# Kernel tuning notes

Measured on AMD Instinct MI355X. Metric: run time of the kernel, lower is better.

The kernel has to match this reference:

```python
import jax, jax.numpy as jnp
import numpy as np

N_NODES = 50000
N_EDGES = 500000
N_GRAPHS = 512


def _segmean(vals, ids, num):
    # avg aggregation: segment mean with safe divide for empty segments
    s = jax.ops.segment_sum(vals, ids, num_segments=num)
    c = jax.ops.segment_sum(jnp.ones((vals.shape[0], 1), vals.dtype), ids, num_segments=num)
    return s / jnp.maximum(c, 1.0)


def setup_inputs() -> dict:
    key = jax.random.key(0)
    ks = iter(jax.random.split(key, 64))

    def nrm(shape, scale=0.05):
        return jax.random.normal(next(ks), shape, dtype=jnp.float32) * scale

    inp = {}
    inp['x'] = nrm((N_NODES, 64), 1.0)
    inp['e'] = nrm((N_EDGES, 32), 1.0)
    inp['u'] = nrm((N_GRAPHS, 64), 1.0)
    inp['a'] = nrm((N_GRAPHS, 8), 1.0)
    inp['senders'] = jax.random.randint(next(ks), (N_EDGES,), 0, N_NODES)
    inp['receivers'] = jax.random.randint(next(ks), (N_EDGES,), 0, N_NODES)
    inp['node_graph'] = jnp.sort(jax.random.randint(next(ks), (N_NODES,), 0, N_GRAPHS))
    inp['edge_graph'] = jnp.sort(jax.random.randint(next(ks), (N_EDGES,), 0, N_GRAPHS))
    # block 1 (hidden 256)
    inp['We1'] = nrm((32, 256)); inp['be1'] = jnp.zeros((256,), jnp.float32)
    inp['Wn1'] = nrm((64, 256)); inp['Win1'] = nrm((256, 256)); inp['Wout1'] = nrm((256, 256)); inp['bn1'] = jnp.zeros((256,), jnp.float32)
    inp['Wg1'] = nrm((64, 256)); inp['Wgn1'] = nrm((256, 256)); inp['Wge1'] = nrm((256, 256)); inp['bg1'] = jnp.zeros((256,), jnp.float32)
    # block 2 (hidden 128)
    inp['We2'] = nrm((256, 128)); inp['be2'] = jnp.zeros((128,), jnp.float32)
    inp['Wn2'] = nrm((256, 128)); inp['Win2'] = nrm((128, 128)); inp['Wout2'] = nrm((128, 128)); inp['bn2'] = jnp.zeros((128,), jnp.float32)
    inp['Wg2'] = nrm((256, 128)); inp['Wgn2'] = nrm((128, 128)); inp['Wge2'] = nrm((128, 128)); inp['bg2'] = jnp.zeros((128,), jnp.float32)
    # global readout (global_features only)
    inp['Wga'] = nrm((128, 128)); inp['bga'] = jnp.zeros((128,), jnp.float32)
    # action-value MLP: (128 + 8) -> 256 -> 256 -> 1
    inp['Wa1'] = nrm((136, 256)); inp['ba1'] = jnp.zeros((256,), jnp.float32)
    inp['Wa2'] = nrm((256, 256)); inp['ba2'] = jnp.zeros((256,), jnp.float32)
    inp['Wa3'] = nrm((256, 1)); inp['ba3'] = jnp.zeros((1,), jnp.float32)
    return inp


def reference(x, e, u, a, senders, receivers, node_graph, edge_graph,
              We1, be1, Wn1, Win1, Wout1, bn1, Wg1, Wgn1, Wge1, bg1,
              We2, be2, Wn2, Win2, Wout2, bn2, Wg2, Wgn2, Wge2, bg2,
              Wga, bga, Wa1, ba1, Wa2, ba2, Wa3, ba3):
    # --- GraphNetwork block 1 (hidden 256) ---
    e1 = jax.nn.relu(e @ We1 + be1)                                  # [E,256]
    inc1 = _segmean(e1, receivers, N_NODES)                          # avg incoming per node
    out1 = _segmean(e1, senders, N_NODES)                            # avg outgoing per node
    n1 = jax.nn.relu(x @ Wn1 + inc1 @ Win1 + out1 @ Wout1 + bn1)     # [N,256]
    u1 = jax.nn.relu(u @ Wg1 + _segmean(n1, node_graph, N_GRAPHS) @ Wgn1
                     + _segmean(e1, edge_graph, N_GRAPHS) @ Wge1 + bg1)  # [B,256]
    # --- GraphNetwork block 2 (hidden 128) ---
    e2 = jax.nn.relu(e1 @ We2 + be2)                                 # [E,128]
    inc2 = _segmean(e2, receivers, N_NODES)
    out2 = _segmean(e2, senders, N_NODES)
    n2 = jax.nn.relu(n1 @ Wn2 + inc2 @ Win2 + out2 @ Wout2 + bn2)    # [N,128]
    u2 = jax.nn.relu(u1 @ Wg2 + _segmean(n2, node_graph, N_GRAPHS) @ Wgn2
                     + _segmean(e2, edge_graph, N_GRAPHS) @ Wge2 + bg2)  # [B,128]
    # --- global readout + action-value MLP ---
    state_value = u2 @ Wga + bga                                     # [B,128]
    h = jnp.concatenate([state_value, a], axis=1)                    # [B,136]
    h = jax.nn.relu(h @ Wa1 + ba1)
    h = jax.nn.relu(h @ Wa2 + ba2)
    return h @ Wa3 + ba3                                             # [B,1]
```

## Files before the change

### kernel.cpp

```cpp
#include <hip/hip_runtime.h>
#include <hip/hip_bf16.h>

#define N_NODES 50000
#define N_EDGES 500000
#define N_GRAPHS 512

#define FXS16 2048.0f
#define FXI16 4.8828125e-4f

__device__ __forceinline__ unsigned long long pk16x4(float4 v) {
    const unsigned long long a = (unsigned int)fmaf(v.x, FXS16, 0.5f);
    const unsigned long long b = (unsigned int)fmaf(v.y, FXS16, 0.5f);
    const unsigned long long c = (unsigned int)fmaf(v.z, FXS16, 0.5f);
    const unsigned long long d = (unsigned int)fmaf(v.w, FXS16, 0.5f);
    return a | (b << 16) | (c << 32) | (d << 48);
}

typedef __attribute__((ext_vector_type(8))) short bf16x8;
typedef __attribute__((ext_vector_type(4))) float f32x4;

__global__ __launch_bounds__(256) void prep_kernel(
    const float* __restrict__ We2,  const float* __restrict__ Wn1,
    const float* __restrict__ Win1, const float* __restrict__ Wout1,
    const float* __restrict__ Wn2,  const float* __restrict__ Win2,
    const float* __restrict__ Wout2, const float* __restrict__ We1,
    __hip_bfloat16* __restrict__ Wt2,  __hip_bfloat16* __restrict__ Wn1t,
    __hip_bfloat16* __restrict__ Win1t,__hip_bfloat16* __restrict__ Wout1t,
    __hip_bfloat16* __restrict__ Wn2t, __hip_bfloat16* __restrict__ Win2t,
    __hip_bfloat16* __restrict__ Wout2t, __hip_bfloat16* __restrict__ We1t)
{
    const int b = blockIdx.x, t = threadIdx.x;
    const float* src; __hip_bfloat16* dst; int K, N, base;
    if (b < 128)      { src = We2;   dst = Wt2;    K = 256; N = 128; base = 0; }
    else if (b < 192) { src = Wn1;   dst = Wn1t;   K = 64;  N = 256; base = 128; }
    else if (b < 448) { src = Win1;  dst = Win1t;  K = 256; N = 256; base = 192; }
    else if (b < 704) { src = Wout1; dst = Wout1t; K = 256; N = 256; base = 448; }
    else if (b < 832) { src = Wn2;   dst = Wn2t;   K = 256; N = 128; base = 704; }
    else if (b < 896) { src = Win2;  dst = Win2t;  K = 128; N = 128; base = 832; }
    else if (b < 960) { src = Wout2; dst = Wout2t; K = 128; N = 128; base = 896; }
    else              { src = We1;   dst = We1t;   K = 32;  N = 256; base = 960; }
    const int i = (b - base) * 256 + t;
    const int n = i / K, k = i - n * K;
    dst[i] = __float2bfloat16(src[(size_t)k * N + n]);
}

__global__ __launch_bounds__(256) void convert_e_kernel(
    const float* __restrict__ e, __hip_bfloat16* __restrict__ ebf)
{
    const long i = (long)blockIdx.x * 256 + threadIdx.x;
    if (i * 8 >= (long)N_EDGES * 32) return;
    const float4 v0 = *(const float4*)&e[i * 8];
    const float4 v1 = *(const float4*)&e[i * 8 + 4];
    __hip_bfloat16* d = &ebf[i * 8];
    *(__hip_bfloat162*)&d[0] = __float22bfloat162_rn(make_float2(v0.x, v0.y));
    *(__hip_bfloat162*)&d[2] = __float22bfloat162_rn(make_float2(v0.z, v0.w));
    *(__hip_bfloat162*)&d[4] = __float22bfloat162_rn(make_float2(v1.x, v1.y));
    *(__hip_bfloat162*)&d[6] = __float22bfloat162_rn(make_float2(v1.z, v1.w));
}


#define NTILES 196

__global__ __launch_bounds__(256) void count_kernel(
    const int* __restrict__ senders, const int* __restrict__ receivers,
    unsigned int* __restrict__ rc, unsigned int* __restrict__ sc)
{
    const int i = blockIdx.x * 256 + threadIdx.x;
    if (i < N_EDGES) {
        atomicAdd(&rc[receivers[i]], 1u);
        atomicAdd(&sc[senders[i]], 1u);
    }
}

__global__ __launch_bounds__(256) void scan_tile_sum(
    const unsigned int* __restrict__ rc, const unsigned int* __restrict__ sc,
    unsigned int* __restrict__ tsR, unsigned int* __restrict__ tsS)
{
    const int b = blockIdx.x;
    const int sel = (b >= NTILES);
    const int tile = sel ? b - NTILES : b;
    const unsigned int* src = sel ? sc : rc;
    unsigned int* ts = sel ? tsS : tsR;
    const int t = threadIdx.x;
    const int i = tile * 256 + t;
    unsigned int v = (i < N_NODES) ? src[i] : 0u;
    __shared__ unsigned int s[256];
    s[t] = v; __syncthreads();
    for (int off = 128; off > 0; off >>= 1) {
        if (t < off) s[t] += s[t + off];
        __syncthreads();
    }
    if (t == 0) ts[tile] = s[0];
}

__global__ __launch_bounds__(256) void scan_tile_offsets(
    unsigned int* __restrict__ tsR, unsigned int* __restrict__ tsS,
    int* __restrict__ roff, int* __restrict__ soff)
{
    __shared__ unsigned int s[256];
    const int t = threadIdx.x;
    for (int sel = 0; sel < 2; sel++) {
        unsigned int* ts = sel ? tsS : tsR;
        int* off = sel ? soff : roff;
        unsigned int v = (t < NTILES) ? ts[t] : 0u;
        s[t] = v; __syncthreads();
        for (int o = 1; o < 256; o <<= 1) {
            unsigned int x = (t >= o) ? s[t - o] : 0u;
            __syncthreads();
            s[t] += x;
            __syncthreads();
        }
        const unsigned int incl = s[t];
        if (t < NTILES) ts[t] = incl - v;
        if (t == NTILES - 1) off[N_NODES] = (int)incl;
        __syncthreads();
    }
}

__global__ __launch_bounds__(256) void scan_finalize(
    const unsigned int* __restrict__ rc, const unsigned int* __restrict__ sc,
    const unsigned int* __restrict__ tsR, const unsigned int* __restrict__ tsS,
    int* __restrict__ roff, int* __restrict__ soff,
    unsigned int* __restrict__ wpR, unsigned int* __restrict__ wpS)
{
    const int b = blockIdx.x;
    const int sel = (b >= NTILES);
    const int tile = sel ? b - NTILES : b;
    const unsigned int* src = sel ? sc : rc;
    const unsigned int* ts = sel ? tsS : tsR;
    int* off = sel ? soff : roff;
    unsigned int* wp = sel ? wpS : wpR;
    const int t = threadIdx.x, i = tile * 256 + t;
    unsigned int v = (i < N_NODES) ? src[i] : 0u;
    __shared__ unsigned int s[256];
    s[t] = v; __syncthreads();
    for (int o = 1; o < 256; o <<= 1) {
        unsigned int x = (t >= o) ? s[t - o] : 0u;
        __syncthreads();
        s[t] += x;
        __syncthreads();
    }
    const unsigned int excl = s[t] - v + ts[tile];
    if (i < N_NODES) { off[i] = (int)excl; wp[i] = excl; }
}

__global__ __launch_bounds__(256) void csr_fill(
    const int* __restrict__ senders, const int* __restrict__ receivers,
    unsigned int* __restrict__ wpR, unsigned int* __restrict__ wpS,
    int* __restrict__ csrR, int* __restrict__ csrS)
{
    const int i = blockIdx.x * 256 + threadIdx.x;
    if (i < N_EDGES) {
        csrR[atomicAdd(&wpR[receivers[i]], 1u)] = i;
        csrS[atomicAdd(&wpS[senders[i]], 1u)] = i;
    }
}

#define EPB 32
#define EBP 40
#define E1P 264
#define E2P 132

__global__ __launch_bounds__(256) void edge_kernel_e2(
    const float* __restrict__ e,
    const int* __restrict__ edge_graph,
    const __hip_bfloat16* __restrict__ We1t, const float* __restrict__ be1,
    const __hip_bfloat16* __restrict__ Wt2,
    const float* __restrict__ be2,
    float* __restrict__ ge1, float* __restrict__ ge2, float* __restrict__ gecnt)
{
    __shared__ __hip_bfloat16 eB[EPB * EBP];
    __shared__ __hip_bfloat16 e1B[EPB * E1P];
    __shared__ float e2L[EPB * E2P];
    __shared__ int gidx[EPB];

    const int t = threadIdx.x;
    const long e0 = (long)blockIdx.x * EPB;

    {
        const int j = t >> 3, c4 = (t & 7) * 4;
        const float4 v = *(const float4*)&e[(e0 + j) * 32 + c4];
        __hip_bfloat16* d = &eB[j * EBP + c4];
        *(__hip_bfloat162*)&d[0] = __float22bfloat162_rn(make_float2(v.x, v.y));
        *(__hip_bfloat162*)&d[2] = __float22bfloat162_rn(make_float2(v.z, v.w));
    }
    if (t < EPB) gidx[t] = edge_graph[e0 + t];
    __syncthreads();

    const int wv = t >> 6, ln = t & 63;
    const int r0 = ln & 15, q = ln >> 4;

    #pragma unroll
    for (int mt = 0; mt < 2; mt++) {
        const bf16x8 a = *(const bf16x8*)&eB[(mt * 16 + r0) * EBP + q * 8];
        #pragma unroll
        for (int nn = 0; nn < 4; nn++) {
            const int n = (wv * 4 + nn) * 16 + r0;
            const bf16x8 wb = *(const bf16x8*)&We1t[(size_t)n * 32 + q * 8];
            f32x4 c = {0.f, 0.f, 0.f, 0.f};
            c = __builtin_amdgcn_mfma_f32_16x16x32_bf16(a, wb, c, 0, 0, 0);
            const float bz = be1[n];
            #pragma unroll
            for (int r = 0; r < 4; r++)
                e1B[(mt * 16 + q * 4 + r) * E1P + n] =
                    __float2bfloat16(fmaxf(c[r] + bz, 0.f));
        }
    }
    __syncthreads();

    {
        f32x4 acc[2][2] = {{{0.f,0.f,0.f,0.f},{0.f,0.f,0.f,0.f}},
                           {{0.f,0.f,0.f,0.f},{0.f,0.f,0.f,0.f}}};
        const int n0 = (2 * wv) * 16 + r0;
        const int n1 = (2 * wv + 1) * 16 + r0;
        #pragma unroll
        for (int kb = 0; kb < 8; kb++) {
            const int k0 = kb * 32 + q * 8;
            const bf16x8 a0 = *(const bf16x8*)&e1B[(r0) * E1P + k0];
            const bf16x8 a1 = *(const bf16x8*)&e1B[(16 + r0) * E1P + k0];
            const bf16x8 b0 = *(const bf16x8*)&Wt2[(size_t)n0 * 256 + k0];
            const bf16x8 b1 = *(const bf16x8*)&Wt2[(size_t)n1 * 256 + k0];
            acc[0][0] = __builtin_amdgcn_mfma_f32_16x16x32_bf16(a0, b0, acc[0][0], 0, 0, 0);
            acc[0][1] = __builtin_amdgcn_mfma_f32_16x16x32_bf16(a0, b1, acc[0][1], 0, 0, 0);
            acc[1][0] = __builtin_amdgcn_mfma_f32_16x16x32_bf16(a1, b0, acc[1][0], 0, 0, 0);
            acc[1][1] = __builtin_amdgcn_mfma_f32_16x16x32_bf16(a1, b1, acc[1][1], 0, 0, 0);
        }
        const float bz0 = be2[2 * wv * 16 + r0];
        const float bz1 = be2[(2 * wv + 1) * 16 + r0];
        #pragma unroll
        for (int mt = 0; mt < 2; mt++) {
            const int m = mt * 16 + q * 4;
            #pragma unroll
            for (int r = 0; r < 4; r++) {
                e2L[(m + r) * E2P + 2 * wv * 16 + r0]       = fmaxf(acc[mt][0][r] + bz0, 0.f);
                e2L[(m + r) * E2P + (2 * wv + 1) * 16 + r0] = fmaxf(acc[mt][1][r] + bz1, 0.f);
            }
        }
    }
    __syncthreads();

    if (gidx[0] == gidx[EPB - 1]) {
        const int g = gidx[0];
        float s = 0.f;
        #pragma unroll
        for (int j = 0; j < EPB; j++) s += __bfloat162float(e1B[j * E1P + t]);
        atomicAdd(&ge1[(size_t)g * 256 + t], s);
        if (t < 128) {
            float s2 = 0.f;
            #pragma unroll
            for (int j = 0; j < EPB; j++) s2 += e2L[j * E2P + t];
            atomicAdd(&ge2[(size_t)g * 128 + t], s2);
        }
        if (t == 0) atomicAdd(&gecnt[g], (float)EPB);
    } else {
        int j = 0;
        while (j < EPB) {
            const int g = gidx[j];
            int j2 = j;
            float s = 0.f;
            while (j2 < EPB && gidx[j2] == g) { s += __bfloat162float(e1B[j2 * E1P + t]); j2++; }
            atomicAdd(&ge1[(size_t)g * 256 + t], s);
            if (t < 128) {
                float s2 = 0.f;
                for (int jj = j; jj < j2; jj++) s2 += e2L[jj * E2P + t];
                atomicAdd(&ge2[(size_t)g * 128 + t], s2);
            }
            if (t == 0) atomicAdd(&gecnt[g], (float)(j2 - j));
            j = j2;
        }
    }
}

#define ANPB 16
#define CHK 32
#define ESP 40
#define E1CP 312
#define E2CP 184
#define JADDR(j, c, P) ((j) * (P) + (c) + ((((j) >> 3) & 3) << 4))

__global__ __launch_bounds__(256) void agg_kernel(
    const __hip_bfloat16* __restrict__ ebf,
    const int* __restrict__ roff, const int* __restrict__ soff,
    const int* __restrict__ csrR, const int* __restrict__ csrS,
    const __hip_bfloat16* __restrict__ We1t, const float* __restrict__ be1,
    const __hip_bfloat16* __restrict__ Wt2, const float* __restrict__ be2,
    __hip_bfloat16* __restrict__ i1d, __hip_bfloat16* __restrict__ o1d,
    __hip_bfloat16* __restrict__ i2d, __hip_bfloat16* __restrict__ o2d)
{
    __shared__ __hip_bfloat16 eS[CHK * ESP];
    __shared__ __hip_bfloat16 e1C[CHK * E1CP];
    __shared__ __hip_bfloat16 e2C[CHK * E2CP];
    __shared__ int idL[CHK];
    __shared__ int segL[CHK];
    __shared__ int offL[ANPB + 1];

    const int t = threadIdx.x;
    int b = blockIdx.x;
    const int side = (b >= (N_NODES / ANPB));
    if (side) b -= N_NODES / ANPB;
    const int n0 = b * ANPB;
    const int* off = side ? soff : roff;
    const int* lst = side ? csrS : csrR;
    __hip_bfloat16* d1 = side ? o1d : i1d;
    __hip_bfloat16* d2 = side ? o2d : i2d;

    if (t <= ANPB) offL[t] = off[n0 + t];
    __syncthreads();
    const int base = offL[0], end = offL[ANPB];

    const int wv = t >> 6, ln = t & 63;
    const int r0 = ln & 15, q = ln >> 4;

    f32x4 s1[4] = {{0.f,0.f,0.f,0.f},{0.f,0.f,0.f,0.f},
                   {0.f,0.f,0.f,0.f},{0.f,0.f,0.f,0.f}};
    f32x4 s2[2] = {{0.f,0.f,0.f,0.f},{0.f,0.f,0.f,0.f}};

    float bz1[4], bz2[2];
    #pragma unroll
    for (int nn = 0; nn < 4; nn++) bz1[nn] = be1[(wv * 4 + nn) * 16 + r0];
    #pragma unroll
    for (int nn = 0; nn < 2; nn++) bz2[nn] = be2[(wv * 2 + nn) * 16 + r0];

    for (int cb = base; cb < end; cb += CHK) {
        const int cnt = min(CHK, end - cb);
        if (t < CHK) {
            int sg = -1;
            if (t < cnt) {
                const int p = cb + t;
                idL[t] = lst[p];
                sg = 0;
                #pragma unroll
                for (int j = 1; j < ANPB; j++) sg += (p >= offL[j]) ? 1 : 0;
            }
            segL[t] = sg;
        }
        __syncthreads();
        if (t < 128) {
            const int sl = t >> 2, cg = (t & 3) * 8;
            bf16x8 v = {0, 0, 0, 0, 0, 0, 0, 0};
            if (sl < cnt) v = *(const bf16x8*)&ebf[(size_t)idL[sl] * 32 + cg];
            *(bf16x8*)&eS[sl * ESP + cg] = v;
        }
        __syncthreads();

        bf16x8 ind;
        #pragma unroll
        for (int i = 0; i < 8; i++)
            ind[i] = (segL[q * 8 + i] == r0) ? (short)0x3F80 : (short)0;

        #pragma unroll
        for (int mt = 0; mt < 2; mt++) {
            const bf16x8 a = *(const bf16x8*)&eS[(mt * 16 + r0) * ESP + q * 8];
            #pragma unroll
            for (int nn = 0; nn < 4; nn++) {
                const int n = (wv * 4 + nn) * 16 + r0;
                const bf16x8 wb = *(const bf16x8*)&We1t[(size_t)n * 32 + q * 8];
                f32x4 c = {0.f, 0.f, 0.f, 0.f};
                c = __builtin_amdgcn_mfma_f32_16x16x32_bf16(a, wb, c, 0, 0, 0);
                #pragma unroll
                for (int r = 0; r < 4; r++)
                    e1C[JADDR(mt * 16 + q * 4 + r, n, E1CP)] =
                        __float2bfloat16(fmaxf(c[r] + bz1[nn], 0.f));
            }
        }
        __syncthreads();

        #pragma unroll
        for (int nn = 0; nn < 4; nn++) {
            const int n = (wv * 4 + nn) * 16 + r0;
            bf16x8 bfr;
            #pragma unroll
            for (int i = 0; i < 8; i++)
                bfr[i] = *(const short*)&e1C[JADDR(q * 8 + i, n, E1CP)];
            s1[nn] = __builtin_amdgcn_mfma_f32_16x16x32_bf16(ind, bfr, s1[nn], 0, 0, 0);
        }

        #pragma unroll
        for (int mt = 0; mt < 2; mt++) {
            f32x4 c[2] = {{0.f,0.f,0.f,0.f},{0.f,0.f,0.f,0.f}};
            #pragma unroll
            for (int ks = 0; ks < 8; ks++) {
                const bf16x8 a = *(const bf16x8*)&e1C[JADDR(mt * 16 + r0, ks * 32 + q * 8, E1CP)];
                #pragma unroll
                for (int nn = 0; nn < 2; nn++) {
                    const int n = (wv * 2 + nn) * 16 + r0;
                    const bf16x8 wb = *(const bf16x8*)&Wt2[(size_t)n * 256 + ks * 32 + q * 8];
                    c[nn] = __builtin_amdgcn_mfma_f32_16x16x32_bf16(a, wb, c[nn], 0, 0, 0);
                }
            }
            #pragma unroll
            for (int nn = 0; nn < 2; nn++) {
                const int n = (wv * 2 + nn) * 16 + r0;
                #pragma unroll
                for (int r = 0; r < 4; r++)
                    e2C[JADDR(mt * 16 + q * 4 + r, n, E2CP)] =
                        __float2bfloat16(fmaxf(c[nn][r] + bz2[nn], 0.f));
            }
        }
        __syncthreads();

        #pragma unroll
        for (int nn = 0; nn < 2; nn++) {
            const int n = (wv * 2 + nn) * 16 + r0;
            bf16x8 bfr;
            #pragma unroll
            for (int i = 0; i < 8; i++)
                bfr[i] = *(const short*)&e2C[JADDR(q * 8 + i, n, E2CP)];
            s2[nn] = __builtin_amdgcn_mfma_f32_16x16x32_bf16(ind, bfr, s2[nn], 0, 0, 0);
        }
        __syncthreads();
    }

    {
        float inv[4];
        #pragma unroll
        for (int r = 0; r < 4; r++) {
            const int m = q * 4 + r;
            const int deg = offL[m + 1] - offL[m];
            inv[r] = 1.f / (float)(deg > 0 ? deg : 1);
        }
        #pragma unroll
        for (int nn = 0; nn < 4; nn++) {
            const int n = (wv * 4 + nn) * 16 + r0;
            #pragma unroll
            for (int r = 0; r < 4; r++)
                e1C[(q * 4 + r) * E1CP + n] = __float2bfloat16(s1[nn][r] * inv[r]);
        }
        #pragma unroll
        for (int nn = 0; nn < 2; nn++) {
            const int n = (wv * 2 + nn) * 16 + r0;
            #pragma unroll
            for (int r = 0; r < 4; r++)
                e2C[(q * 4 + r) * E2CP + n] = __float2bfloat16(s2[nn][r] * inv[r]);
        }
    }
    __syncthreads();
    for (int i = t; i < ANPB * 32; i += 256) {
        const int j = i >> 5, c8 = (i & 31) * 8;
        *(bf16x8*)&d1[(size_t)(n0 + j) * 256 + c8] = *(const bf16x8*)&e1C[j * E1CP + c8];
    }
    for (int i = t; i < ANPB * 16; i += 256) {
        const int j = i >> 4, c8 = (i & 15) * 8;
        *(bf16x8*)&d2[(size_t)(n0 + j) * 128 + c8] = *(const bf16x8*)&e2C[j * E2CP + c8];
    }
}

#define NPB 16
#define XP  72
#define K1P 264
#define K2P 136

__global__ __launch_bounds__(256) void node_kernel_dense(
    const float* __restrict__ x,
    const int* __restrict__ node_graph,
    const __hip_bfloat16* __restrict__ i1d, const __hip_bfloat16* __restrict__ o1d,
    const __hip_bfloat16* __restrict__ i2d, const __hip_bfloat16* __restrict__ o2d,
    const __hip_bfloat16* __restrict__ Wn1t, const __hip_bfloat16* __restrict__ Win1t,
    const __hip_bfloat16* __restrict__ Wout1t, const float* __restrict__ bn1,
    const __hip_bfloat16* __restrict__ Wn2t, const __hip_bfloat16* __restrict__ Win2t,
    const __hip_bfloat16* __restrict__ Wout2t, const float* __restrict__ bn2,
    float* __restrict__ gn1, float* __restrict__ gn2, float* __restrict__ gncnt)
{
    __shared__ __hip_bfloat16 xB[NPB * XP];
    __shared__ __hip_bfloat16 i1B[NPB * K1P];
    __shared__ __hip_bfloat16 o1B[NPB * K1P];
    __shared__ __hip_bfloat16 i2B[NPB * K2P];
    __shared__ __hip_bfloat16 o2B[NPB * K2P];
    __shared__ __hip_bfloat16 n1B[NPB * K1P];
    __shared__ __hip_bfloat16 n2B[NPB * K2P];
    __shared__ int gI[NPB];

    const int t = threadIdx.x;
    const long n0 = (long)blockIdx.x * NPB;

    if (t < NPB) gI[t] = node_graph[n0 + t];
    for (int i = t; i < NPB * 16; i += 256) {
        const int j = i >> 4, c4 = (i & 15) * 4;
        const float4 v = *(const float4*)&x[(n0 + j) * 64 + c4];
        *(__hip_bfloat162*)&xB[j * XP + c4]     = __float22bfloat162_rn(make_float2(v.x, v.y));
        *(__hip_bfloat162*)&xB[j * XP + c4 + 2] = __float22bfloat162_rn(make_float2(v.z, v.w));
    }
    for (int i = t; i < NPB * 32; i += 256) {
        const int j = i >> 5, c8 = (i & 31) * 8;
        *(bf16x8*)&i1B[j * K1P + c8] = *(const bf16x8*)&i1d[(size_t)(n0 + j) * 256 + c8];
        *(bf16x8*)&o1B[j * K1P + c8] = *(const bf16x8*)&o1d[(size_t)(n0 + j) * 256 + c8];
    }
    for (int i = t; i < NPB * 16; i += 256) {
        const int j = i >> 4, c8 = (i & 15) * 8;
        *(bf16x8*)&i2B[j * K2P + c8] = *(const bf16x8*)&i2d[(size_t)(n0 + j) * 128 + c8];
        *(bf16x8*)&o2B[j * K2P + c8] = *(const bf16x8*)&o2d[(size_t)(n0 + j) * 128 + c8];
    }
    __syncthreads();

    const int wv = t >> 6, ln = t & 63;
    const int r0 = ln & 15, q = ln >> 4;

    {
        f32x4 acc[4] = {{0.f,0.f,0.f,0.f},{0.f,0.f,0.f,0.f},
                        {0.f,0.f,0.f,0.f},{0.f,0.f,0.f,0.f}};
        #pragma unroll
        for (int ks = 0; ks < 2; ks++) {
            const int k0 = ks * 32 + q * 8;
            const bf16x8 a = *(const bf16x8*)&xB[r0 * XP + k0];
            #pragma unroll
            for (int nn = 0; nn < 4; nn++) {
                const int n = (wv * 4 + nn) * 16 + r0;
                const bf16x8 b = *(const bf16x8*)&Wn1t[(size_t)n * 64 + k0];
                acc[nn] = __builtin_amdgcn_mfma_f32_16x16x32_bf16(a, b, acc[nn], 0, 0, 0);
            }
        }
        #pragma unroll
        for (int ks = 0; ks < 8; ks++) {
            const int k0 = ks * 32 + q * 8;
            const bf16x8 a = *(const bf16x8*)&i1B[r0 * K1P + k0];
            #pragma unroll
            for (int nn = 0; nn < 4; nn++) {
                const int n = (wv * 4 + nn) * 16 + r0;
                const bf16x8 b = *(const bf16x8*)&Win1t[(size_t)n * 256 + k0];
                acc[nn] = __builtin_amdgcn_mfma_f32_16x16x32_bf16(a, b, acc[nn], 0, 0, 0);
            }
        }
        #pragma unroll
        for (int ks = 0; ks < 8; ks++) {
            const int k0 = ks * 32 + q * 8;
            const bf16x8 a = *(const bf16x8*)&o1B[r0 * K1P + k0];
            #pragma unroll
            for (int nn = 0; nn < 4; nn++) {
                const int n = (wv * 4 + nn) * 16 + r0;
                const bf16x8 b = *(const bf16x8*)&Wout1t[(size_t)n * 256 + k0];
                acc[nn] = __builtin_amdgcn_mfma_f32_16x16x32_bf16(a, b, acc[nn], 0, 0, 0);
            }
        }
        #pragma unroll
        for (int nn = 0; nn < 4; nn++) {
            const int n = (wv * 4 + nn) * 16 + r0;
            const float bz = bn1[n];
            #pragma unroll
            for (int r = 0; r < 4; r++) {
                const int m = q * 4 + r;
                n1B[m * K1P + n] = __float2bfloat16(fmaxf(acc[nn][r] + bz, 0.f));
            }
        }
    }
    __syncthreads();

    if (gI[0] == gI[NPB - 1]) {
        float s = 0.f;
        #pragma unroll
        for (int j = 0; j < NPB; j++) s += __bfloat162float(n1B[j * K1P + t]);
        atomicAdd(&gn1[(size_t)gI[0] * 256 + t], s);
        if (t == 0) atomicAdd(&gncnt[gI[0]], (float)NPB);
    } else {
        int j = 0;
        while (j < NPB) {
            const int g = gI[j];
            int j2 = j;
            float s = 0.f;
            while (j2 < NPB && gI[j2] == g) { s += __bfloat162float(n1B[j2 * K1P + t]); j2++; }
            atomicAdd(&gn1[(size_t)g * 256 + t], s);
            if (t == 0) atomicAdd(&gncnt[g], (float)(j2 - j));
            j = j2;
        }
    }

    {
        f32x4 acc[2] = {{0.f,0.f,0.f,0.f},{0.f,0.f,0.f,0.f}};
        #pragma unroll
        for (int ks = 0; ks < 8; ks++) {
            const int k0 = ks * 32 + q * 8;
            const bf16x8 a = *(const bf16x8*)&n1B[r0 * K1P + k0];
            #pragma unroll
            for (int nn = 0; nn < 2; nn++) {
                const int n = (wv * 2 + nn) * 16 + r0;
                const bf16x8 b = *(const bf16x8*)&Wn2t[(size_t)n * 256 + k0];
                acc[nn] = __builtin_amdgcn_mfma_f32_16x16x32_bf16(a, b, acc[nn], 0, 0, 0);
            }
        }
        #pragma unroll
        for (int ks = 0; ks < 4; ks++) {
            const int k0 = ks * 32 + q * 8;
            const bf16x8 a = *(const bf16x8*)&i2B[r0 * K2P + k0];
            #pragma unroll
            for (int nn = 0; nn < 2; nn++) {
                const int n = (wv * 2 + nn) * 16 + r0;
                const bf16x8 b = *(const bf16x8*)&Win2t[(size_t)n * 128 + k0];
                acc[nn] = __builtin_amdgcn_mfma_f32_16x16x32_bf16(a, b, acc[nn], 0, 0, 0);
            }
        }
        #pragma unroll
        for (int ks = 0; ks < 4; ks++) {
            const int k0 = ks * 32 + q * 8;
            const bf16x8 a = *(const bf16x8*)&o2B[r0 * K2P + k0];
            #pragma unroll
            for (int nn = 0; nn < 2; nn++) {
                const int n = (wv * 2 + nn) * 16 + r0;
                const bf16x8 b = *(const bf16x8*)&Wout2t[(size_t)n * 128 + k0];
                acc[nn] = __builtin_amdgcn_mfma_f32_16x16x32_bf16(a, b, acc[nn], 0, 0, 0);
            }
        }
        #pragma unroll
        for (int nn = 0; nn < 2; nn++) {
            const int n = (wv * 2 + nn) * 16 + r0;
            const float bz = bn2[n];
            #pragma unroll
            for (int r = 0; r < 4; r++) {
                const int m = q * 4 + r;
                n2B[m * K2P + n] = __float2bfloat16(fmaxf(acc[nn][r] + bz, 0.f));
            }
        }
    }
    __syncthreads();

    if (t < 128) {
        if (gI[0] == gI[NPB - 1]) {
            float s = 0.f;
            #pragma unroll
            for (int j = 0; j < NPB; j++) s += __bfloat162float(n2B[j * K2P + t]);
            atomicAdd(&gn2[(size_t)gI[0] * 128 + t], s);
        } else {
            int j = 0;
            while (j < NPB) {
                const int g = gI[j];
                int j2 = j;
                float s = 0.f;
                while (j2 < NPB && gI[j2] == g) { s += __bfloat162float(n2B[j2 * K2P + t]); j2++; }
                atomicAdd(&gn2[(size_t)g * 128 + t], s);
                j = j2;
            }
        }
    }
}

__global__ __launch_bounds__(256) void graph_kernel(
    const float* __restrict__ u,
    const float* __restrict__ a,
    const float* __restrict__ ge1, const float* __restrict__ ge2,
    const float* __restrict__ gecnt,
    const float* __restrict__ gn1, const float* __restrict__ gn2,
    const float* __restrict__ gncnt,
    const float* __restrict__ Wg1, const float* __restrict__ Wgn1,
    const float* __restrict__ Wge1, const float* __restrict__ bg1,
    const float* __restrict__ Wg2, const float* __restrict__ Wgn2,
    const float* __restrict__ Wge2, const float* __restrict__ bg2,
    const float* __restrict__ Wga, const float* __restrict__ bga,
    const float* __restrict__ Wa1, const float* __restrict__ ba1,
    const float* __restrict__ Wa2, const float* __restrict__ ba2,
    const float* __restrict__ Wa3, const float* __restrict__ ba3,
    float* __restrict__ out)
{
    const int g = blockIdx.x;
    const int t = threadIdx.x;
    __shared__ float uL[64], mn1[256], me1[256], mn2[128], me2[128];
    __shared__ float u1L[256], u2L[128], hL[144], h1L[256], h2L[256];
    __shared__ float red[4];

    const float ec = 1.f / fmaxf(gecnt[g], 1.f);
    const float nc = 1.f / fmaxf(gncnt[g], 1.f);
    if (t < 64) uL[t] = u[(size_t)g * 64 + t];
    mn1[t] = gn1[(size_t)g * 256 + t] * nc;
    me1[t] = ge1[(size_t)g * 256 + t] * ec;
    if (t < 128) {
        mn2[t] = gn2[(size_t)g * 128 + t] * nc;
        me2[t] = ge2[(size_t)g * 128 + t] * ec;
    }
    if (t >= 136 && t < 144) hL[t] = 0.f;
    __syncthreads();

    {
        float acc = bg1[t];
        for (int k = 0; k < 64; k++)  acc = fmaf(uL[k],  Wg1[(size_t)k * 256 + t], acc);
        for (int k = 0; k < 256; k++) acc = fmaf(mn1[k], Wgn1[(size_t)k * 256 + t], acc);
        for (int k = 0; k < 256; k++) acc = fmaf(me1[k], Wge1[(size_t)k * 256 + t], acc);
        u1L[t] = fmaxf(acc, 0.f);
    }
    __syncthreads();
    if (t < 128) {
        float acc = bg2[t];
        for (int k = 0; k < 256; k++) acc = fmaf(u1L[k], Wg2[(size_t)k * 128 + t], acc);
        for (int k = 0; k < 128; k++) acc = fmaf(mn2[k], Wgn2[(size_t)k * 128 + t], acc);
        for (int k = 0; k < 128; k++) acc = fmaf(me2[k], Wge2[(size_t)k * 128 + t], acc);
        u2L[t] = fmaxf(acc, 0.f);
    }
    __syncthreads();
    if (t < 128) {
        float acc = bga[t];
        for (int k = 0; k < 128; k++) acc = fmaf(u2L[k], Wga[(size_t)k * 128 + t], acc);
        hL[t] = acc;
    }
    if (t >= 128 && t < 136) hL[t] = a[(size_t)g * 8 + (t - 128)];
    __syncthreads();
    {
        float acc = ba1[t];
        for (int k = 0; k < 136; k++) acc = fmaf(hL[k], Wa1[(size_t)k * 256 + t], acc);
        h1L[t] = fmaxf(acc, 0.f);
    }
    __syncthreads();
    {
        float acc = ba2[t];
        for (int k = 0; k < 256; k++) acc = fmaf(h1L[k], Wa2[(size_t)k * 256 + t], acc);
        h2L[t] = fmaxf(acc, 0.f);
    }
    __syncthreads();
    {
        float p = h2L[t] * Wa3[t];
        for (int off = 32; off > 0; off >>= 1) p += __shfl_down(p, off, 64);
        if ((t & 63) == 0) red[t >> 6] = p;
        __syncthreads();
        if (t == 0) out[g] = red[0] + red[1] + red[2] + red[3] + ba3[0];
    }
}


__global__ __launch_bounds__(256) void edge_kernel(
// ... 520 lines not shown
```

Baseline: 920.7 us.

## Double-buffer edge gather and widen aggregation chunk to 64 edges

The aggregation kernel now processes 64 edges per chunk instead of 32. It double-buffers the edge ids, segment ids and gathered edge features, so the global gather for the next chunk is issued while the current chunk's MFMA work runs. This is meant to hide global-load latency and cut the number of barriers per edge. In exchange it uses more LDS (the e1C/e2C buffers double in size), which may lower occupancy. Nodes with few edges also waste more of each chunk on padding.

```diff
diff --git a/kernel.cpp b/kernel.cpp
--- a/kernel.cpp
+++ b/kernel.cpp
@@ -272,7 +272,7 @@
 }
 
 #define ANPB 16
-#define CHK 32
+#define CHK 64
 #define ESP 40
 #define E1CP 312
 #define E2CP 184
@@ -287,11 +287,11 @@
     __hip_bfloat16* __restrict__ i1d, __hip_bfloat16* __restrict__ o1d,
     __hip_bfloat16* __restrict__ i2d, __hip_bfloat16* __restrict__ o2d)
 {
-    __shared__ __hip_bfloat16 eS[CHK * ESP];
+    __shared__ __hip_bfloat16 eS[2][CHK * ESP];
     __shared__ __hip_bfloat16 e1C[CHK * E1CP];
     __shared__ __hip_bfloat16 e2C[CHK * E2CP];
-    __shared__ int idL[CHK];
-    __shared__ int segL[CHK];
+    __shared__ int idL[2][CHK];
+    __shared__ int segL[2][CHK];
     __shared__ int offL[ANPB + 1];
 
     const int t = threadIdx.x;
@@ -307,9 +307,11 @@
     if (t <= ANPB) offL[t] = off[n0 + t];
     __syncthreads();
     const int base = offL[0], end = offL[ANPB];
+    const int nchunks = (end - base + CHK - 1) / CHK;
 
     const int wv = t >> 6, ln = t & 63;
     const int r0 = ln & 15, q = ln >> 4;
+    const int srow = t >> 2, scol = (t & 3) * 8;
 
     f32x4 s1[4] = {{0.f,0.f,0.f,0.f},{0.f,0.f,0.f,0.f},
                    {0.f,0.f,0.f,0.f},{0.f,0.f,0.f,0.f}};
@@ -321,63 +323,85 @@
     #pragma unroll
     for (int nn = 0; nn < 2; nn++) bz2[nn] = be2[(wv * 2 + nn) * 16 + r0];
 
-    for (int cb = base; cb < end; cb += CHK) {
-        const int cnt = min(CHK, end - cb);
+    if (t < CHK) {
+        const int p = base + t;
+        int sg = -1, id = 0;
+        if (p < end) {
+            id = lst[p];
+            sg = 0;
+            #pragma unroll
+            for (int j = 1; j < ANPB; j++) sg += (p >= offL[j]) ? 1 : 0;
+        }
+        idL[0][t] = id; segL[0][t] = sg;
+    }
+    __syncthreads();
+    {
+        bf16x8 v = {0, 0, 0, 0, 0, 0, 0, 0};
+        if (segL[0][srow] >= 0) v = *(const bf16x8*)&ebf[(size_t)idL[0][srow] * 32 + scol];
+        *(bf16x8*)&eS[0][srow * ESP + scol] = v;
+    }
+    __syncthreads();
+
+    int cur = 0;
+    for (int c = 0; c < nchunks; c++) {
+        const int nxt = cur ^ 1;
+
+        int idn = 0, sgn = -1;
         if (t < CHK) {
-            int sg = -1;
-            if (t < cnt) {
-                const int p = cb + t;
-                idL[t] = lst[p];
-                sg = 0;
+            const int p = base + (c + 1) * CHK + t;
+            if (c + 1 < nchunks && p < end) {
+                idn = lst[p];
+                sgn = 0;
                 #pragma unroll
-                for (int j = 1; j < ANPB; j++) sg += (p >= offL[j]) ? 1 : 0;
-            }
-            segL[t] = sg;
-        }
-        __syncthreads();
-        if (t < 128) {
-            const int sl = t >> 2, cg = (t & 3) * 8;
-            bf16x8 v = {0, 0, 0, 0, 0, 0, 0, 0};
-            if (sl < cnt) v = *(const bf16x8*)&ebf[(size_t)idL[sl] * 32 + cg];
-            *(bf16x8*)&eS[sl * ESP + cg] = v;
-        }
-        __syncthreads();
-
-        bf16x8 ind;
-        #pragma unroll
-        for (int i = 0; i < 8; i++)
-            ind[i] = (segL[q * 8 + i] == r0) ? (short)0x3F80 : (short)0;
-
-        #pragma unroll
-        for (int mt = 0; mt < 2; mt++) {
-            const bf16x8 a = *(const bf16x8*)&eS[(mt * 16 + r0) * ESP + q * 8];
+                for (int j = 1; j < ANPB; j++) sgn += (p >= offL[j]) ? 1 : 0;
+            }
+        }
+
+        bf16x8 ind[2];
+        #pragma unroll
+        for (int ks = 0; ks < 2; ks++)
+            #pragma unroll
+            for (int i = 0; i < 8; i++)
+                ind[ks][i] = (segL[cur][ks * 32 + q * 8 + i] == r0) ? (short)0x3F80 : (short)0;
+
+        #pragma unroll
+        for (int mt = 0; mt < 4; mt++) {
+            const bf16x8 a = *(const bf16x8*)&eS[cur][(mt * 16 + r0) * ESP + q * 8];
             #pragma unroll
             for (int nn = 0; nn < 4; nn++) {
                 const int n = (wv * 4 + nn) * 16 + r0;
                 const bf16x8 wb = *(const bf16x8*)&We1t[(size_t)n * 32 + q * 8];
-                f32x4 c = {0.f, 0.f, 0.f, 0.f};
-                c = __builtin_amdgcn_mfma_f32_16x16x32_bf16(a, wb, c, 0, 0, 0);
+                f32x4 cc = {0.f, 0.f, 0.f, 0.f};
+                cc = __builtin_amdgcn_mfma_f32_16x16x32_bf16(a, wb, cc, 0, 0, 0);
                 #pragma unroll
                 for (int r = 0; r < 4; r++)
                     e1C[JADDR(mt * 16 + q * 4 + r, n, E1CP)] =
-                        __float2bfloat16(fmaxf(c[r] + bz1[nn], 0.f));
-            }
-        }
+                        __float2bfloat16(fmaxf(cc[r] + bz1[nn], 0.f));
+            }
+        }
+        if (t < CHK) { idL[nxt][t] = idn; segL[nxt][t] = sgn; }
         __syncthreads();
 
-        #pragma unroll
-        for (int nn = 0; nn < 4; nn++) {
-            const int n = (wv * 4 + nn) * 16 + r0;
-            bf16x8 bfr;
-            #pragma unroll
-            for (int i = 0; i < 8; i++)
-                bfr[i] = *(const short*)&e1C[JADDR(q * 8 + i, n, E1CP)];
-            s1[nn] = __builtin_amdgcn_mfma_f32_16x16x32_bf16(ind, bfr, s1[nn], 0, 0, 0);
-        }
-
-        #pragma unroll
-        for (int mt = 0; mt < 2; mt++) {
-            f32x4 c[2] = {{0.f,0.f,0.f,0.f},{0.f,0.f,0.f,0.f}};
+        bf16x8 pre = {0, 0, 0, 0, 0, 0, 0, 0};
+        if (segL[nxt][srow] >= 0)
+            pre = *(const bf16x8*)&ebf[(size_t)idL[nxt][srow] * 32 + scol];
+
+        #pragma unroll
+        for (int ks = 0; ks < 2; ks++) {
+            #pragma unroll
+            for (int nn = 0; nn < 4; nn++) {
+                const int n = (wv * 4 + nn) * 16 + r0;
+                bf16x8 bfr;
+                #pragma unroll
+                for (int i = 0; i < 8; i++)
+                    bfr[i] = *(const short*)&e1C[JADDR(ks * 32 + q * 8 + i, n, E1CP)];
+                s1[nn] = __builtin_amdgcn_mfma_f32_16x16x32_bf16(ind[ks], bfr, s1[nn], 0, 0, 0);
+            }
+        }
+
+        #pragma unroll
+        for (int mt = 0; mt < 4; mt++) {
+            f32x4 cc[2] = {{0.f,0.f,0.f,0.f},{0.f,0.f,0.f,0.f}};
             #pragma unroll
             for (int ks = 0; ks < 8; ks++) {
                 const bf16x8 a = *(const bf16x8*)&e1C[JADDR(mt * 16 + r0, ks * 32 + q * 8, E1CP)];
@@ -385,7 +409,7 @@
                 for (int nn = 0; nn < 2; nn++) {
                     const int n = (wv * 2 + nn) * 16 + r0;
                     const bf16x8 wb = *(const bf16x8*)&Wt2[(size_t)n * 256 + ks * 32 + q * 8];
-                    c[nn] = __builtin_amdgcn_mfma_f32_16x16x32_bf16(a, wb, c[nn], 0, 0, 0);
+                    cc[nn] = __builtin_amdgcn_mfma_f32_16x16x32_bf16(a, wb, cc[nn], 0, 0, 0);
                 }
             }
             #pragma unroll
@@ -394,21 +418,27 @@
                 #pragma unroll
                 for (int r = 0; r < 4; r++)
                     e2C[JADDR(mt * 16 + q * 4 + r, n, E2CP)] =
-                        __float2bfloat16(fmaxf(c[nn][r] + bz2[nn], 0.f));
+                        __float2bfloat16(fmaxf(cc[nn][r] + bz2[nn], 0.f));
             }
         }
         __syncthreads();
 
         #pragma unroll
-        for (int nn = 0; nn < 2; nn++) {
-            const int n = (wv * 2 + nn) * 16 + r0;
-            bf16x8 bfr;
-            #pragma unroll
-            for (int i = 0; i < 8; i++)
-                bfr[i] = *(const short*)&e2C[JADDR(q * 8 + i, n, E2CP)];
-            s2[nn] = __builtin_amdgcn_mfma_f32_16x16x32_bf16(ind, bfr, s2[nn], 0, 0, 0);
-        }
+        for (int ks = 0; ks < 2; ks++) {
+            #pragma unroll
+            for (int nn = 0; nn < 2; nn++) {
+                const int n = (wv * 2 + nn) * 16 + r0;
+                bf16x8 bfr;
+                #pragma unroll
+                for (int i = 0; i < 8; i++)
+                    bfr[i] = *(const short*)&e2C[JADDR(ks * 32 + q * 8 + i, n, E2CP)];
+                s2[nn] = __builtin_amdgcn_mfma_f32_16x16x32_bf16(ind[ks], bfr, s2[nn], 0, 0, 0);
+            }
+        }
+
+        *(bf16x8*)&eS[nxt][srow * ESP + scol] = pre;
         __syncthreads();
+        cur = nxt;
     }
 
     {
```

Result: no change. 902.8 us, median of 2 (-1.9%).
